# Kernel optimization log

Measured on AMD Instinct MI355X. Metric: run time of the kernel, lower is better.

## Reference

```python
import jax, jax.numpy as jnp
import numpy as np

N_NODES = 50000
N_EDGES = 800000
IN_DIM = 128
HID = 256
B_SEEDS = 8192
EPS = 1e-12


def _sage_layer(h, src, dst, Wn, Ws, b):
    # mean-aggregation SAGEConv: fc_self(h) + fc_neigh(mean over in-neighbors)
    msgs = h[src]  # [E, d]
    agg = jax.ops.segment_sum(msgs, dst, num_segments=N_NODES)
    cnt = jax.ops.segment_sum(jnp.ones((src.shape[0], 1), h.dtype), dst, num_segments=N_NODES)
    neigh = agg / jnp.maximum(cnt, 1.0)
    return neigh @ Wn + h @ Ws + b


def _sage(x, src, dst, Wn1, Ws1, b1, Wn2, Ws2, b2):
    h = jax.nn.relu(_sage_layer(x, src, dst, Wn1, Ws1, b1))
    return _sage_layer(h, src, dst, Wn2, Ws2, b2)


def _l2norm(x):
    # F.normalize(p=2, dim=1)
    n = jnp.sqrt(jnp.sum(x * x, axis=1, keepdims=True))
    return x / jnp.maximum(n, EPS)


def _unique_gather(h, ids):
    # torch.unique(ids, return_inverse=True) then h[inverse]
    uniq, inv = jnp.unique(ids, return_inverse=True, size=ids.shape[0], fill_value=0)
    return h[uniq][inv]


def setup_inputs() -> dict:
    key = jax.random.key(0)
    ks = jax.random.split(key, 16)
    s = lambda d: 1.0 / np.sqrt(d)
    return {
        "x_i": jax.random.normal(ks[0], (N_NODES, IN_DIM), jnp.float32),
        "x_j": jax.random.normal(ks[1], (N_NODES, IN_DIM), jnp.float32),
        "src_i": jax.random.randint(ks[2], (N_EDGES,), 0, N_NODES, jnp.int32),
        "dst_i": jax.random.randint(ks[3], (N_EDGES,), 0, N_NODES, jnp.int32),
        "src_j": jax.random.randint(ks[4], (N_EDGES,), 0, N_NODES, jnp.int32),
        "dst_j": jax.random.randint(ks[5], (N_EDGES,), 0, N_NODES, jnp.int32),
        "ids_i": jax.random.randint(ks[6], (B_SEEDS,), 0, N_NODES, jnp.int32),
        "ids_j": jax.random.randint(ks[7], (B_SEEDS,), 0, N_NODES, jnp.int32),
        "Wn1": jax.random.normal(ks[8], (IN_DIM, HID), jnp.float32) * s(IN_DIM),
        "Ws1": jax.random.normal(ks[9], (IN_DIM, HID), jnp.float32) * s(IN_DIM),
        "b1": jnp.zeros((HID,), jnp.float32),
        "Wn2": jax.random.normal(ks[10], (HID, HID), jnp.float32) * s(HID),
        "Ws2": jax.random.normal(ks[11], (HID, HID), jnp.float32) * s(HID),
        "b2": jnp.zeros((HID,), jnp.float32),
        "W_out": jax.random.normal(ks[12], (2 * HID, 1), jnp.float32) * s(2 * HID),
        "b_out": jnp.zeros((1,), jnp.float32),
    }


def reference(x_i, x_j, src_i, dst_i, src_j, dst_j, ids_i, ids_j,
              Wn1, Ws1, b1, Wn2, Ws2, b2, W_out, b_out):
    sage_o_i = _l2norm(_sage(x_i, src_i, dst_i, Wn1, Ws1, b1, Wn2, Ws2, b2))
    sage_o_j = _l2norm(_sage(x_j, src_j, dst_j, Wn1, Ws1, b1, Wn2, Ws2, b2))
    g_i = _unique_gather(sage_o_i, ids_i)  # [B, HID]
    g_j = _unique_gather(sage_o_j, ids_j)
    h_cur = jnp.concatenate([g_i, g_j], axis=-1) @ W_out + b_out  # [B, 1]
    return jnp.stack([h_cur.squeeze(-1)])  # [1, B]
```

## Files before the change

### kernel.cpp

```cpp
#include <hip/hip_runtime.h>

constexpr int NN = 50000;
constexpr int NE = 800000;
constexpr int IND = 128;
constexpr int HD = 256;
constexpr int BS = 8192;
constexpr int NPAD = 50176;
constexpr int NBKT = 196;
constexpr int BCAP = 8192;

typedef __attribute__((ext_vector_type(8))) short short8v;
typedef __attribute__((ext_vector_type(4))) float floatx4;

__device__ inline ushort f2b(float f) {
  unsigned u = __float_as_uint(f);
  unsigned r = (u + 0x7fffu + ((u >> 16) & 1u)) >> 16;
  return (ushort)r;
}
__device__ inline float b2f(ushort b) {
  return __uint_as_float((unsigned)b << 16);
}
__device__ __forceinline__ void acc2(unsigned u, float& a0, float& a1) {
  a0 += __uint_as_float(u << 16);
  a1 += __uint_as_float(u & 0xffff0000u);
}
__device__ inline int wave_incl_scan(int x, int lane) {
#pragma unroll
  for (int d = 1; d < 64; d <<= 1) {
    int y = __shfl_up(x, d);
    if (lane >= d) x += y;
  }
  return x;
}

__device__ __forceinline__ void gload16(const ushort* g, ushort* l) {
  __builtin_amdgcn_global_load_lds(
      (const __attribute__((address_space(1))) void*)g,
      (__attribute__((address_space(3))) void*)l, 16, 0, 0);
}

__global__ __launch_bounds__(256) void k_bin(const int* __restrict__ src_i,
                                             const int* __restrict__ dst_i,
                                             const int* __restrict__ src_j,
                                             const int* __restrict__ dst_j,
                                             int* __restrict__ bcnt,
                                             int* __restrict__ bucketbuf) {
  __shared__ int hist[NBKT], gbase[NBKT], lcur[NBKT];
  const int blk = blockIdx.x;
  const int g = blk >= 98;
  const int c = blk - g * 98;
  const int* src = g ? src_j : src_i;
  const int* dst = g ? dst_j : dst_i;
  const int t = threadIdx.x;
  if (t < NBKT) hist[t] = 0;
  __syncthreads();
  const int e0 = c * 8192;
#pragma unroll
  for (int k = 0; k < 32; ++k) {
    int e = e0 + k * 256 + t;
    if (e < NE) atomicAdd(&hist[dst[e] >> 8], 1);
  }
  __syncthreads();
  if (t < NBKT) {
    int h = hist[t];
    gbase[t] = h ? atomicAdd(&bcnt[g * NBKT + t], h) : 0;
    lcur[t] = 0;
  }
  __syncthreads();
#pragma unroll
  for (int k = 0; k < 32; ++k) {
    int e = e0 + k * 256 + t;
    if (e < NE) {
      int d = dst[e];
      int b = d >> 8;
      int p = gbase[b] + atomicAdd(&lcur[b], 1);
      if (p < BCAP)
        bucketbuf[(g * NBKT + b) * BCAP + p] = (src[e] << 8) | (d & 255);
    }
  }
}

__global__ __launch_bounds__(256) void k_bktscan(const int* __restrict__ bcnt,
                                                 int* __restrict__ bktbase) {
  __shared__ int wt[4];
  __shared__ int carry, tot;
  const int t = threadIdx.x, lane = t & 63;
  if (t == 0) carry = 0;
  __syncthreads();
  for (int ch = 0; ch < 2; ++ch) {
    int i = ch * 256 + t;
    int v = (i < 2 * NBKT) ? min(bcnt[i], BCAP) : 0;
    int x = wave_incl_scan(v, lane);
    if (lane == 63) wt[t >> 6] = x;
    __syncthreads();
    if (t == 0) {
      int run = 0;
#pragma unroll
      for (int j = 0; j < 4; ++j) { int tv = wt[j]; wt[j] = run; run += tv; }
      tot = run;
    }
    __syncthreads();
    if (i < 2 * NBKT) bktbase[i] = carry + x - v + wt[t >> 6];
    __syncthreads();
    if (t == 0) carry += tot;
    __syncthreads();
  }
}

__global__ __launch_bounds__(256) void k_build(const int* __restrict__ bucketbuf,
                                               const int* __restrict__ bcnt,
                                               const int* __restrict__ bktbase,
                                               int* __restrict__ csr,
                                               int* __restrict__ cnt2,
                                               int* __restrict__ row_start2) {
  __shared__ int hist[256], lstart[256], lcur[256];
  __shared__ int stage[BCAP];
  __shared__ int wt[4];
  const int b = blockIdx.x;
  const int g = b >= NBKT;
  const int bb = b - g * NBKT;
  const int t = threadIdx.x, lane = t & 63;
  const int C = min(bcnt[b], BCAP);
  const int base = bktbase[b];
  const int* buf = bucketbuf + b * BCAP;
  hist[t] = 0;
  __syncthreads();
  for (int i = t; i < C; i += 256) atomicAdd(&hist[buf[i] & 255], 1);
  __syncthreads();
  int v = hist[t];
  int x = wave_incl_scan(v, lane);
  if (lane == 63) wt[t >> 6] = x;
  __syncthreads();
  if (t == 0) {
    int run = 0;
#pragma unroll
    for (int j = 0; j < 4; ++j) { int tv = wt[j]; wt[j] = run; run += tv; }
  }
  __syncthreads();
  int ls = x - v + wt[t >> 6];
  lstart[t] = ls;
  lcur[t] = ls;
  __syncthreads();
  for (int i = t; i < C; i += 256) {
    int val = buf[i];
    int p = atomicAdd(&lcur[val & 255], 1);
    stage[p] = val >> 8;
  }
  __syncthreads();
  for (int i = t; i < C; i += 256) csr[base + i] = stage[i];
  int node = bb * 256 + t;
  cnt2[g * NPAD + node] = v;
  row_start2[g * NPAD + node] = base + ls;
}

__global__ __launch_bounds__(256) void k_tobf16(const float* __restrict__ x_i,
                                                const float* __restrict__ x_j,
                                                ushort* __restrict__ xb2) {
  int i = blockIdx.x * 256 + threadIdx.x;
  int e4 = i * 4;
  int g = e4 >= NN * IND;
  const float* xp = g ? x_j : x_i;
  float4 v = *(const float4*)(xp + (e4 - g * NN * IND));
  ushort4 u;
  u.x = f2b(v.x); u.y = f2b(v.y); u.z = f2b(v.z); u.w = f2b(v.w);
  *(ushort4*)(xb2 + e4) = u;
}

__global__ __launch_bounds__(256) void k_wt(const float* __restrict__ Wn1,
                                            const float* __restrict__ Ws1,
                                            ushort* __restrict__ Wt) {
  int i = blockIdx.x * 256 + threadIdx.x;
  int n = i >> 8, k = i & 255;
  float v = (k < 128) ? Wn1[k * HD + n] : Ws1[(k - 128) * HD + n];
  Wt[n * 256 + k] = f2b(v);
}

__global__ __launch_bounds__(256) void k_w2(const float* __restrict__ Wn2,
                                            const float* __restrict__ Ws2,
                                            ushort* __restrict__ Whi,
                                            ushort* __restrict__ Wlo) {
  int i = blockIdx.x * 256 + threadIdx.x;
  int n = i >> 9, k = i & 511;
  float v = (k < 256) ? Wn2[k * HD + n] : Ws2[(k - 256) * HD + n];
  ushort hi = f2b(v);
  Whi[n * 512 + k] = hi;
  Wlo[n * 512 + k] = f2b(v - b2f(hi));
}

__global__ __launch_bounds__(256) void k_agg1(const ushort* __restrict__ xb2,
                                              const int* __restrict__ csr,
                                              const int* __restrict__ row_start2,
                                              const int* __restrict__ cnt2,
                                              ushort* __restrict__ aggb2) {
  int w = threadIdx.x >> 6, l = threadIdx.x & 63;
  int n = blockIdx.x * 4 + w;
  int g = n >= NN;
  int nl = n - g * NN;
  int st = row_start2[g * NPAD + nl], deg = cnt2[g * NPAD + nl];
  const ushort* xb = xb2 + g * NN * IND;
  float a0 = 0.f, a1 = 0.f;
  int e = 0;
  for (; e + 8 <= deg; e += 8) {
    int s0 = csr[st + e + 0], s1 = csr[st + e + 1];
    int s2 = csr[st + e + 2], s3 = csr[st + e + 3];
    int s4 = csr[st + e + 4], s5 = csr[st + e + 5];
    int s6 = csr[st + e + 6], s7 = csr[st + e + 7];
    unsigned u0 = *(const unsigned*)(xb + s0 * IND + 2 * l);
    unsigned u1 = *(const unsigned*)(xb + s1 * IND + 2 * l);
    unsigned u2 = *(const unsigned*)(xb + s2 * IND + 2 * l);
    unsigned u3 = *(const unsigned*)(xb + s3 * IND + 2 * l);
    unsigned u4 = *(const unsigned*)(xb + s4 * IND + 2 * l);
    unsigned u5 = *(const unsigned*)(xb + s5 * IND + 2 * l);
    unsigned u6 = *(const unsigned*)(xb + s6 * IND + 2 * l);
    unsigned u7 = *(const unsigned*)(xb + s7 * IND + 2 * l);
    acc2(u0, a0, a1); acc2(u1, a0, a1); acc2(u2, a0, a1); acc2(u3, a0, a1);
    acc2(u4, a0, a1); acc2(u5, a0, a1); acc2(u6, a0, a1); acc2(u7, a0, a1);
  }
  for (; e + 4 <= deg; e += 4) {
    int s0 = csr[st + e + 0], s1 = csr[st + e + 1];
    int s2 = csr[st + e + 2], s3 = csr[st + e + 3];
    unsigned u0 = *(const unsigned*)(xb + s0 * IND + 2 * l);
    unsigned u1 = *(const unsigned*)(xb + s1 * IND + 2 * l);
    unsigned u2 = *(const unsigned*)(xb + s2 * IND + 2 * l);
    unsigned u3 = *(const unsigned*)(xb + s3 * IND + 2 * l);
    acc2(u0, a0, a1); acc2(u1, a0, a1); acc2(u2, a0, a1); acc2(u3, a0, a1);
  }
  for (; e < deg; ++e) {
    int s = csr[st + e];
    unsigned u = *(const unsigned*)(xb + s * IND + 2 * l);
    acc2(u, a0, a1);
  }
  float inv = 1.f / (float)max(deg, 1);
  ushort2 u;
  u.x = f2b(a0 * inv);
  u.y = f2b(a1 * inv);
  *(ushort2*)(aggb2 + (g * NN + nl) * IND + 2 * l) = u;
}

__global__ __launch_bounds__(256) void k_gemm1(const ushort* __restrict__ aggb2,
                                               const ushort* __restrict__ xb2,
                                               const ushort* __restrict__ Wt,
                                               const float* __restrict__ b1,
                                               ushort* __restrict__ h1b2) {
  __shared__ ushort smem[16384];
  const int t = threadIdx.x;
  const int g = blockIdx.x >= 392;
  const int row0 = (blockIdx.x - g * 392) * 128, col0 = blockIdx.y * 128;
  const ushort* aggb = aggb2 + g * NN * IND;
  const ushort* xb = xb2 + g * NN * IND;
  ushort* h1b = h1b2 + g * NN * HD;
  const int w = t >> 6, l = t & 63;
  const int wm = w & 1, wn = w >> 1;

  const int r0 = t >> 2, cs0 = t & 3;
  const int c0 = cs0 ^ (r0 & 3);
  const int rA0 = min(row0 + r0, NN - 1);
  const int rA1 = min(row0 + r0 + 64, NN - 1);
  const int gA0 = rA0 * IND + c0 * 8;
  const int gA1 = rA1 * IND + c0 * 8;
  const int gB0 = (col0 + r0) * 256 + c0 * 8;
  const int gB1 = (col0 + r0 + 64) * 256 + c0 * 8;
  const int wofs = w * 512;

  floatx4 acc[4][4];
#pragma unroll
  for (int i = 0; i < 4; ++i)
#pragma unroll
    for (int j = 0; j < 4; ++j) acc[i][j] = (floatx4){0.f, 0.f, 0.f, 0.f};

#define STAGE(buf, kk)                                                      \
  do {                                                                      \
    const ushort* Ab = ((kk) < 128) ? (aggb + (kk)) : (xb + ((kk) - 128));  \
    ushort* Ald = smem + (buf) * 4096;                                      \
    ushort* Bld = smem + 8192 + (buf) * 4096;                               \
    gload16(Ab + gA0, Ald + wofs);                                          \
    gload16(Ab + gA1, Ald + 2048 + wofs);                                   \
    gload16(Wt + gB0 + (kk), Bld + wofs);                                   \
    gload16(Wt + gB1 + (kk), Bld + 2048 + wofs);                            \
  } while (0)

  STAGE(0, 0);
  __syncthreads();
  int cur = 0;
  const int rA = l & 15, gg = l >> 4;
  for (int step = 0; step < 8; ++step) {
    if (step < 7) STAGE(cur ^ 1, (step + 1) * 32);
    const ushort* Abuf = smem + cur * 4096;
    const ushort* Bbuf = smem + 8192 + cur * 4096;
    short8v af[4], bf[4];
#pragma unroll
    for (int i = 0; i < 4; ++i) {
      int r = wm * 64 + i * 16 + rA;
      af[i] = *(const short8v*)(Abuf + r * 32 + ((gg ^ (r & 3)) * 8));
    }
#pragma unroll
    for (int j = 0; j < 4; ++j) {
      int r = wn * 64 + j * 16 + rA;
      bf[j] = *(const short8v*)(Bbuf + r * 32 + ((gg ^ (r & 3)) * 8));
    }
#pragma unroll
    for (int i = 0; i < 4; ++i)
#pragma unroll
      for (int j = 0; j < 4; ++j)
        acc[i][j] = __builtin_amdgcn_mfma_f32_16x16x32_bf16(af[i], bf[j],
                                                            acc[i][j], 0, 0, 0);
    if (step < 7) {
      __syncthreads();
      cur ^= 1;
    }
  }
#undef STAGE

  __syncthreads();
  const int rD = l >> 4, cD = l & 15;
#pragma unroll
  for (int j = 0; j < 4; ++j) {
    int cl = wn * 64 + j * 16 + cD;
    float bias = b1[col0 + cl];
#pragma unroll
    for (int i = 0; i < 4; ++i) {
      int rbase = wm * 64 + i * 16 + rD * 4;
#pragma unroll
      for (int rr = 0; rr < 4; ++rr)
        smem[(rbase + rr) * 128 + cl] = f2b(fmaxf(acc[i][j][rr] + bias, 0.f));
    }
  }
  __syncthreads();
  const int rl = t >> 4, ch = t & 15;
#pragma unroll
  for (int it = 0; it < 8; ++it) {
    int row_l = rl + it * 16;
    int grow = row0 + row_l;
    if (grow < NN)
      *(short8v*)(h1b + grow * HD + col0 + ch * 8) =
          *(const short8v*)(smem + row_l * 128 + ch * 8);
  }
}

__global__ __launch_bounds__(256) void k_agg2(
    const ushort* __restrict__ h1b2, const int* __restrict__ csr,
    const int* __restrict__ row_start2, const int* __restrict__ cnt2,
    const int* __restrict__ ids_i, const int* __restrict__ ids_j,
    ushort* __restrict__ A2) {
  __shared__ float red[4][HD];
  const int b = blockIdx.x;
  const int g = b >= BS;
  const int node = (g ? ids_j : ids_i)[b - g * BS];
  const int st = row_start2[g * NPAD + node], deg = cnt2[g * NPAD + node];
  const ushort* h1b = h1b2 + g * NN * HD;
  const int w = threadIdx.x >> 6, l = threadIdx.x & 63;
  float a0 = 0.f, a1 = 0.f, a2 = 0.f, a3 = 0.f;
  int e = w;
  for (; e + 4 < deg; e += 8) {
    int sa = csr[st + e], sb = csr[st + e + 4];
    uint2 ua = *(const uint2*)(h1b + sa * HD + l * 4);
    uint2 ub = *(const uint2*)(h1b + sb * HD + l * 4);
    acc2(ua.x, a0, a1); acc2(ua.y, a2, a3);
    acc2(ub.x, a0, a1); acc2(ub.y, a2, a3);
  }
  if (e < deg) {
    int sa = csr[st + e];
    uint2 ua = *(const uint2*)(h1b + sa * HD + l * 4);
    acc2(ua.x, a0, a1); acc2(ua.y, a2, a3);
  }
  red[w][l * 4 + 0] = a0;
  red[w][l * 4 + 1] = a1;
  red[w][l * 4 + 2] = a2;
  red[w][l * 4 + 3] = a3;
  __syncthreads();
  const int t = threadIdx.x;
  float s = (red[0][t] + red[1][t]) + (red[2][t] + red[3][t]);
  s *= 1.f / (float)max(deg, 1);
  A2[b * 512 + t] = f2b(s);
  A2[b * 512 + 256 + t] = h1b[node * HD + t];
}

__global__ __launch_bounds__(256) void k_head(const ushort* __restrict__ A2,
                                              const ushort* __restrict__ Whi,
                                              const ushort* __restrict__ Wlo,
                                              const float* __restrict__ b2,
                                              float* __restrict__ h2) {
  __shared__ ushort Ahl[64 * 32];
  __shared__ ushort Bhl[128 * 32];
  __shared__ ushort Bll[128 * 32];
  const int t = threadIdx.x;
  const int row0 = blockIdx.x * 64, col0 = blockIdx.y * 128;
  const int w = t >> 6, l = t & 63;
  const int wm = w & 1, wn = w >> 1;
  floatx4 acc[2][4];
#pragma unroll
  for (int i = 0; i < 2; ++i)
#pragma unroll
    for (int j = 0; j < 4; ++j) acc[i][j] = (floatx4){0.f, 0.f, 0.f, 0.f};

  for (int kk = 0; kk < 512; kk += 32) {
    if (t < 256) {
      int r = t >> 2, c = t & 3;
      int sw = (c ^ (r & 3)) * 8;
      *(short8v*)(Ahl + r * 32 + sw) =
          *(const short8v*)(A2 + (row0 + r) * 512 + kk + c * 8);
    }
#pragma unroll
    for (int s = t; s < 512; s += 256) {
      int r = s >> 2, c = s & 3;
      int sw = (c ^ (r & 3)) * 8;
      *(short8v*)(Bhl + r * 32 + sw) =
          *(const short8v*)(Whi + (col0 + r) * 512 + kk + c * 8);
      *(short8v*)(Bll + r * 32 + sw) =
          *(const short8v*)(Wlo + (col0 + r) * 512 + kk + c * 8);
    }
    __syncthreads();
    const int rA = l & 15, gg = l >> 4;
    short8v ah[2], bh[4], bl[4];
#pragma unroll
    for (int i = 0; i < 2; ++i) {
      int r = wm * 32 + i * 16 + rA;
      ah[i] = *(const short8v*)(Ahl + r * 32 + ((gg ^ (r & 3)) * 8));
    }
#pragma unroll
    for (int j = 0; j < 4; ++j) {
      int r = wn * 64 + j * 16 + rA;
      int sw = (gg ^ (r & 3)) * 8;
      bh[j] = *(const short8v*)(Bhl + r * 32 + sw);
      bl[j] = *(const short8v*)(Bll + r * 32 + sw);
    }
#pragma unroll
    for (int i = 0; i < 2; ++i)
#pragma unroll
      for (int j = 0; j < 4; ++j) {
        acc[i][j] = __builtin_amdgcn_mfma_f32_16x16x32_bf16(ah[i], bh[j],
                                                            acc[i][j], 0, 0, 0);
        acc[i][j] = __builtin_amdgcn_mfma_f32_16x16x32_bf16(ah[i], bl[j],
                                                            acc[i][j], 0, 0, 0);
      }
    __syncthreads();
  }
  const int rD = l >> 4, cD = l & 15;
#pragma unroll
  for (int j = 0; j < 4; ++j) {
    int col = col0 + wn * 64 + j * 16 + cD;
    float bias = b2[col];
#pragma unroll
    for (int i = 0; i < 2; ++i) {
      int rbase = row0 + wm * 32 + i * 16 + rD * 4;
#pragma unroll
      for (int rr = 0; rr < 4; ++rr) {
        h2[(rbase + rr) * HD + col] = acc[i][j][rr] + bias;
      }
    }
  }
}

__global__ __launch_bounds__(256) void k_out(const float* __restrict__ h2,
                                             const float* __restrict__ W_out,
                                             const float* __restrict__ b_out,
                                             float* __restrict__ out) {
  int w = threadIdx.x >> 6, l = threadIdx.x & 63;
  int s = blockIdx.x * 4 + w;
  float4 vi = *(const float4*)(h2 + s * HD + l * 4);
  float4 vj = *(const float4*)(h2 + (s + BS) * HD + l * 4);
  float4 wi = *(const float4*)(W_out + l * 4);
  float4 wj = *(const float4*)(W_out + 256 + l * 4);
  float ssi = vi.x * vi.x + vi.y * vi.y + vi.z * vi.z + vi.w * vi.w;
  float dpi = vi.x * wi.x + vi.y * wi.y + vi.z * wi.z + vi.w * wi.w;
  float ssj = vj.x * vj.x + vj.y * vj.y + vj.z * vj.z + vj.w * vj.w;
  float dpj = vj.x * wj.x + vj.y * wj.y + vj.z * wj.z + vj.w * wj.w;
#pragma unroll
  for (int o = 32; o; o >>= 1) {
    ssi += __shfl_down(ssi, o);
    dpi += __shfl_down(dpi, o);
    ssj += __shfl_down(ssj, o);
    dpj += __shfl_down(dpj, o);
  }
  if (l == 0) {
    out[s] = dpi / fmaxf(sqrtf(ssi), 1e-12f) +
             dpj / fmaxf(sqrtf(ssj), 1e-12f) + b_out[0];
  }
}

extern "C" void kernel_launch(void* const* d_in, const int* in_sizes, int n_in,
                              void* d_out, int out_size, void* d_ws,
                              size_t ws_size, hipStream_t stream) {
  (void)in_sizes; (void)n_in; (void)out_size; (void)ws_size;
  const float* x_i = (const float*)d_in[0];
  const float* x_j = (const float*)d_in[1];
  const int* src_i = (const int*)d_in[2];
  const int* dst_i = (const int*)d_in[3];
  const int* src_j = (const int*)d_in[4];
  const int* dst_j = (const int*)d_in[5];
  const int* ids_i = (const int*)d_in[6];
  const int* ids_j = (const int*)d_in[7];
  const float* Wn1 = (const float*)d_in[8];
  const float* Ws1 = (const float*)d_in[9];
  const float* b1 = (const float*)d_in[10];
  const float* Wn2 = (const float*)d_in[11];
  const float* Ws2 = (const float*)d_in[12];
  const float* b2 = (const float*)d_in[13];
  const float* W_out = (const float*)d_in[14];
  const float* b_out = (const float*)d_in[15];
  float* out = (float*)d_out;

  char* w = (char*)d_ws;
  int* bcnt       = (int*)(w + 0);
  int* bktbase    = (int*)(w + 2048);
  int* cnt2       = (int*)(w + 4096);
  int* row_start2 = (int*)(w + 405504);
  int* bucketbuf  = (int*)(w + 806912);
  ushort* Wt      = (ushort*)(w + 13651968);
  ushort* W2hi    = (ushort*)(w + 13783040);
  ushort* W2lo    = (ushort*)(w + 14045184);
  ushort* xb2     = (ushort*)(w + 14307328);
  ushort* aggb2   = (ushort*)(w + 39907328);
  ushort* h1b2    = (ushort*)(w + 65507328);
  int* csr        = (int*)(w + 116707328);
  ushort* A2      = (ushort*)(w + 14307328);
  float* h2       = (float*)(w + 31084544);

  k_wt<<<256, 256, 0, stream>>>(Wn1, Ws1, Wt);
  k_w2<<<512, 256, 0, stream>>>(Wn2, Ws2, W2hi, W2lo);
  hipMemsetAsync(bcnt, 0, 2 * NBKT * sizeof(int), stream);
  k_bin<<<196, 256, 0, stream>>>(src_i, dst_i, src_j, dst_j, bcnt, bucketbuf);
  k_bktscan<<<1, 256, 0, stream>>>(bcnt, bktbase);
  k_build<<<392, 256, 0, stream>>>(bucketbuf, bcnt, bktbase, csr, cnt2,
                                   row_start2);
  k_tobf16<<<12500, 256, 0, stream>>>(x_i, x_j, xb2);
  k_agg1<<<25000, 256, 0, stream>>>(xb2, csr, row_start2, cnt2, aggb2);
  k_gemm1<<<dim3(784, 2), 256, 0, stream>>>(aggb2, xb2, Wt, b1, h1b2);
  k_agg2<<<2 * BS, 256, 0, stream>>>(h1b2, csr, row_start2, cnt2, ids_i, ids_j,
                                     A2);
  k_head<<<dim3(256, 2), 256, 0, stream>>>(A2, W2hi, W2lo, b2, h2);
  k_out<<<2048, 256, 0, stream>>>(h2, W_out, b_out, out);
}
```

Measured before the change: 211.5 us.

## Fuse weight prep kernels, pair nodes per wave in agg1, fuse L2-norm+output into head GEMM

Merges the two weight-conversion kernels and the bucket memset into one prep launch. Layer-1 aggregation now has each wave handle two nodes, interleaving their gathers so more loads are in flight. The head GEMM now covers all 256 columns per block, so it can compute the L2 norm and the W_out dot product in its epilogue instead of writing h2 and reading it back in a separate kernel. A small kernel then sums the i and j halves. This trades fewer launches and less h2 traffic for a larger per-block tile (more registers and LDS) and only 256 head blocks.

```diff
diff --git a/kernel.cpp b/kernel.cpp
--- a/kernel.cpp
+++ b/kernel.cpp
@@ -37,6 +37,32 @@
   __builtin_amdgcn_global_load_lds(
       (const __attribute__((address_space(1))) void*)g,
       (__attribute__((address_space(3))) void*)l, 16, 0, 0);
+}
+
+__global__ __launch_bounds__(256) void k_prep(const float* __restrict__ Wn1,
+                                              const float* __restrict__ Ws1,
+                                              const float* __restrict__ Wn2,
+                                              const float* __restrict__ Ws2,
+                                              ushort* __restrict__ Wt,
+                                              ushort* __restrict__ Whi,
+                                              ushort* __restrict__ Wlo,
+                                              int* __restrict__ bcnt) {
+  const int b = blockIdx.x, t = threadIdx.x;
+  if (b < 256) {
+    int i = b * 256 + t;
+    int n = i >> 8, k = i & 255;
+    float v = (k < 128) ? Wn1[k * HD + n] : Ws1[(k - 128) * HD + n];
+    Wt[n * 256 + k] = f2b(v);
+  } else if (b < 768) {
+    int i = (b - 256) * 256 + t;
+    int n = i >> 9, k = i & 511;
+    float v = (k < 256) ? Wn2[k * HD + n] : Ws2[(k - 256) * HD + n];
+    ushort hi = f2b(v);
+    Whi[n * 512 + k] = hi;
+    Wlo[n * 512 + k] = f2b(v - b2f(hi));
+  } else {
+    for (int i = t; i < 2 * NBKT; i += 256) bcnt[i] = 0;
+  }
 }
 
 __global__ __launch_bounds__(256) void k_bin(const int* __restrict__ src_i,
@@ -166,75 +192,79 @@
   *(ushort4*)(xb2 + e4) = u;
 }
 
-__global__ __launch_bounds__(256) void k_wt(const float* __restrict__ Wn1,
-                                            const float* __restrict__ Ws1,
-                                            ushort* __restrict__ Wt) {
-  int i = blockIdx.x * 256 + threadIdx.x;
-  int n = i >> 8, k = i & 255;
-  float v = (k < 128) ? Wn1[k * HD + n] : Ws1[(k - 128) * HD + n];
-  Wt[n * 256 + k] = f2b(v);
-}
-
-__global__ __launch_bounds__(256) void k_w2(const float* __restrict__ Wn2,
-                                            const float* __restrict__ Ws2,
-                                            ushort* __restrict__ Whi,
-                                            ushort* __restrict__ Wlo) {
-  int i = blockIdx.x * 256 + threadIdx.x;
-  int n = i >> 9, k = i & 511;
-  float v = (k < 256) ? Wn2[k * HD + n] : Ws2[(k - 256) * HD + n];
-  ushort hi = f2b(v);
-  Whi[n * 512 + k] = hi;
-  Wlo[n * 512 + k] = f2b(v - b2f(hi));
-}
-
 __global__ __launch_bounds__(256) void k_agg1(const ushort* __restrict__ xb2,
                                               const int* __restrict__ csr,
                                               const int* __restrict__ row_start2,
                                               const int* __restrict__ cnt2,
                                               ushort* __restrict__ aggb2) {
   int w = threadIdx.x >> 6, l = threadIdx.x & 63;
-  int n = blockIdx.x * 4 + w;
-  int g = n >= NN;
-  int nl = n - g * NN;
-  int st = row_start2[g * NPAD + nl], deg = cnt2[g * NPAD + nl];
+  int p = blockIdx.x * 4 + w;
+  int nA = p * 2;
+  int g = nA >= NN;
+  int nl = nA - g * NN;
+  int base = g * NPAD + nl;
+  int stA = row_start2[base], degA = cnt2[base];
+  int stB = row_start2[base + 1], degB = cnt2[base + 1];
   const ushort* xb = xb2 + g * NN * IND;
-  float a0 = 0.f, a1 = 0.f;
+  float a0A = 0.f, a1A = 0.f, a0B = 0.f, a1B = 0.f;
+  int cmn = min(degA, degB);
   int e = 0;
-  for (; e + 8 <= deg; e += 8) {
-    int s0 = csr[st + e + 0], s1 = csr[st + e + 1];
-    int s2 = csr[st + e + 2], s3 = csr[st + e + 3];
-    int s4 = csr[st + e + 4], s5 = csr[st + e + 5];
-    int s6 = csr[st + e + 6], s7 = csr[st + e + 7];
+  for (; e + 4 <= cmn; e += 4) {
+    int sA0 = csr[stA + e + 0], sA1 = csr[stA + e + 1];
+    int sA2 = csr[stA + e + 2], sA3 = csr[stA + e + 3];
+    int sB0 = csr[stB + e + 0], sB1 = csr[stB + e + 1];
+    int sB2 = csr[stB + e + 2], sB3 = csr[stB + e + 3];
+    unsigned uA0 = *(const unsigned*)(xb + sA0 * IND + 2 * l);
+    unsigned uA1 = *(const unsigned*)(xb + sA1 * IND + 2 * l);
+    unsigned uA2 = *(const unsigned*)(xb + sA2 * IND + 2 * l);
+    unsigned uA3 = *(const unsigned*)(xb + sA3 * IND + 2 * l);
+    unsigned uB0 = *(const unsigned*)(xb + sB0 * IND + 2 * l);
+    unsigned uB1 = *(const unsigned*)(xb + sB1 * IND + 2 * l);
+    unsigned uB2 = *(const unsigned*)(xb + sB2 * IND + 2 * l);
+    unsigned uB3 = *(const unsigned*)(xb + sB3 * IND + 2 * l);
+    acc2(uA0, a0A, a1A); acc2(uA1, a0A, a1A);
+    acc2(uA2, a0A, a1A); acc2(uA3, a0A, a1A);
+    acc2(uB0, a0B, a1B); acc2(uB1, a0B, a1B);
+    acc2(uB2, a0B, a1B); acc2(uB3, a0B, a1B);
+  }
+  int eA = e, eB = e;
+  for (; eA + 4 <= degA; eA += 4) {
+    int s0 = csr[stA + eA + 0], s1 = csr[stA + eA + 1];
+    int s2 = csr[stA + eA + 2], s3 = csr[stA + eA + 3];
     unsigned u0 = *(const unsigned*)(xb + s0 * IND + 2 * l);
     unsigned u1 = *(const unsigned*)(xb + s1 * IND + 2 * l);
     unsigned u2 = *(const unsigned*)(xb + s2 * IND + 2 * l);
     unsigned u3 = *(const unsigned*)(xb + s3 * IND + 2 * l);
-    unsigned u4 = *(const unsigned*)(xb + s4 * IND + 2 * l);
-    unsigned u5 = *(const unsigned*)(xb + s5 * IND + 2 * l);
-    unsigned u6 = *(const unsigned*)(xb + s6 * IND + 2 * l);
-    unsigned u7 = *(const unsigned*)(xb + s7 * IND + 2 * l);
-    acc2(u0, a0, a1); acc2(u1, a0, a1); acc2(u2, a0, a1); acc2(u3, a0, a1);
-    acc2(u4, a0, a1); acc2(u5, a0, a1); acc2(u6, a0, a1); acc2(u7, a0, a1);
-  }
-  for (; e + 4 <= deg; e += 4) {
-    int s0 = csr[st + e + 0], s1 = csr[st + e + 1];
-    int s2 = csr[st + e + 2], s3 = csr[st + e + 3];
+    acc2(u0, a0A, a1A); acc2(u1, a0A, a1A);
+    acc2(u2, a0A, a1A); acc2(u3, a0A, a1A);
+  }
+  for (; eA < degA; ++eA) {
+    int s = csr[stA + eA];
+    unsigned u = *(const unsigned*)(xb + s * IND + 2 * l);
+    acc2(u, a0A, a1A);
+  }
+  for (; eB + 4 <= degB; eB += 4) {
+    int s0 = csr[stB + eB + 0], s1 = csr[stB + eB + 1];
+    int s2 = csr[stB + eB + 2], s3 = csr[stB + eB + 3];
     unsigned u0 = *(const unsigned*)(xb + s0 * IND + 2 * l);
     unsigned u1 = *(const unsigned*)(xb + s1 * IND + 2 * l);
     unsigned u2 = *(const unsigned*)(xb + s2 * IND + 2 * l);
     unsigned u3 = *(const unsigned*)(xb + s3 * IND + 2 * l);
-    acc2(u0, a0, a1); acc2(u1, a0, a1); acc2(u2, a0, a1); acc2(u3, a0, a1);
-  }
-  for (; e < deg; ++e) {
-    int s = csr[st + e];
+    acc2(u0, a0B, a1B); acc2(u1, a0B, a1B);
+    acc2(u2, a0B, a1B); acc2(u3, a0B, a1B);
+  }
+  for (; eB < degB; ++eB) {
+    int s = csr[stB + eB];
     unsigned u = *(const unsigned*)(xb + s * IND + 2 * l);
-    acc2(u, a0, a1);
-  }
-  float inv = 1.f / (float)max(deg, 1);
-  ushort2 u;
-  u.x = f2b(a0 * inv);
-  u.y = f2b(a1 * inv);
-  *(ushort2*)(aggb2 + (g * NN + nl) * IND + 2 * l) = u;
+    acc2(u, a0B, a1B);
+  }
+  float invA = 1.f / (float)max(degA, 1);
+  float invB = 1.f / (float)max(degB, 1);
+  ushort2 uA, uB;
+  uA.x = f2b(a0A * invA); uA.y = f2b(a1A * invA);
+  uB.x = f2b(a0B * invB); uB.y = f2b(a1B * invB);
+  *(ushort2*)(aggb2 + (g * NN + nl) * IND + 2 * l) = uA;
+  *(ushort2*)(aggb2 + (g * NN + nl + 1) * IND + 2 * l) = uB;
 }
 
 __global__ __launch_bounds__(256) void k_gemm1(const ushort* __restrict__ aggb2,
@@ -379,103 +409,107 @@
                                               const ushort* __restrict__ Whi,
                                               const ushort* __restrict__ Wlo,
                                               const float* __restrict__ b2,
-                                              float* __restrict__ h2) {
+                                              const float* __restrict__ W_out,
+                                              float* __restrict__ outP) {
   __shared__ ushort Ahl[64 * 32];
-  __shared__ ushort Bhl[128 * 32];
-  __shared__ ushort Bll[128 * 32];
+  __shared__ ushort Bhl[256 * 32];
+  __shared__ ushort Bll[256 * 32];
+  __shared__ float sred[4][64][2];
   const int t = threadIdx.x;
-  const int row0 = blockIdx.x * 64, col0 = blockIdx.y * 128;
+  const int row0 = blockIdx.x * 64;
   const int w = t >> 6, l = t & 63;
-  const int wm = w & 1, wn = w >> 1;
-  floatx4 acc[2][4];
-#pragma unroll
-  for (int i = 0; i < 2; ++i)
+  const int woff = (row0 >= BS) ? 256 : 0;
+  floatx4 acc[4][4];
+#pragma unroll
+  for (int i = 0; i < 4; ++i)
 #pragma unroll
     for (int j = 0; j < 4; ++j) acc[i][j] = (floatx4){0.f, 0.f, 0.f, 0.f};
 
   for (int kk = 0; kk < 512; kk += 32) {
-    if (t < 256) {
+    {
       int r = t >> 2, c = t & 3;
       int sw = (c ^ (r & 3)) * 8;
       *(short8v*)(Ahl + r * 32 + sw) =
           *(const short8v*)(A2 + (row0 + r) * 512 + kk + c * 8);
     }
 #pragma unroll
-    for (int s = t; s < 512; s += 256) {
+    for (int s = t; s < 1024; s += 256) {
       int r = s >> 2, c = s & 3;
       int sw = (c ^ (r & 3)) * 8;
       *(short8v*)(Bhl + r * 32 + sw) =
-          *(const short8v*)(Whi + (col0 + r) * 512 + kk + c * 8);
+          *(const short8v*)(Whi + r * 512 + kk + c * 8);
       *(short8v*)(Bll + r * 32 + sw) =
-          *(const short8v*)(Wlo + (col0 + r) * 512 + kk + c * 8);
+          *(const short8v*)(Wlo + r * 512 + kk + c * 8);
     }
     __syncthreads();
     const int rA = l & 15, gg = l >> 4;
-    short8v ah[2], bh[4], bl[4];
-#pragma unroll
-    for (int i = 0; i < 2; ++i) {
-      int r = wm * 32 + i * 16 + rA;
-      ah[i] = *(const short8v*)(Ahl + r * 32 + ((gg ^ (r & 3)) * 8));
+    short8v af[4], bh[4], bl[4];
+#pragma unroll
+    for (int i = 0; i < 4; ++i) {
+      int r = i * 16 + rA;
+      af[i] = *(const short8v*)(Ahl + r * 32 + ((gg ^ (r & 3)) * 8));
     }
 #pragma unroll
     for (int j = 0; j < 4; ++j) {
-      int r = wn * 64 + j * 16 + rA;
+      int r = w * 64 + j * 16 + rA;
       int sw = (gg ^ (r & 3)) * 8;
       bh[j] = *(const short8v*)(Bhl + r * 32 + sw);
       bl[j] = *(const short8v*)(Bll + r * 32 + sw);
     }
 #pragma unroll
-    for (int i = 0; i < 2; ++i)
+    for (int i = 0; i < 4; ++i)
 #pragma unroll
       for (int j = 0; j < 4; ++j) {
-        acc[i][j] = __builtin_amdgcn_mfma_f32_16x16x32_bf16(ah[i], bh[j],
+        acc[i][j] = __builtin_amdgcn_mfma_f32_16x16x32_bf16(af[i], bh[j],
                                                             acc[i][j], 0, 0, 0);
-        acc[i][j] = __builtin_amdgcn_mfma_f32_16x16x32_bf16(ah[i], bl[j],
+        acc[i][j] = __builtin_amdgcn_mfma_f32_16x16x32_bf16(af[i], bl[j],
                                                             acc[i][j], 0, 0, 0);
       }
     __syncthreads();
   }
-  const int rD = l >> 4, cD = l & 15;
+  const int cD = l & 15, rD = l >> 4;
+  float bj[4], wo[4];
 #pragma unroll
   for (int j = 0; j < 4; ++j) {
-    int col = col0 + wn * 64 + j * 16 + cD;
-    float bias = b2[col];
-#pragma unroll
-    for (int i = 0; i < 2; ++i) {
-      int rbase = row0 + wm * 32 + i * 16 + rD * 4;
-#pragma unroll
-      for (int rr = 0; rr < 4; ++rr) {
-        h2[(rbase + rr) * HD + col] = acc[i][j][rr] + bias;
+    int col = w * 64 + j * 16 + cD;
+    bj[j] = b2[col];
+    wo[j] = W_out[woff + col];
+  }
+#pragma unroll
+  for (int i = 0; i < 4; ++i)
+#pragma unroll
+    for (int rr = 0; rr < 4; ++rr) {
+      float ssv = 0.f, dpv = 0.f;
+#pragma unroll
+      for (int j = 0; j < 4; ++j) {
+        float v = acc[i][j][rr] + bj[j];
+        ssv += v * v;
+        dpv += v * wo[j];
       }
-    }
-  }
-}
-
-__global__ __launch_bounds__(256) void k_out(const float* __restrict__ h2,
-                                             const float* __restrict__ W_out,
-                                             const float* __restrict__ b_out,
-                                             float* __restrict__ out) {
-  int w = threadIdx.x >> 6, l = threadIdx.x & 63;
-  int s = blockIdx.x * 4 + w;
-  float4 vi = *(const float4*)(h2 + s * HD + l * 4);
-  float4 vj = *(const float4*)(h2 + (s + BS) * HD + l * 4);
-  float4 wi = *(const float4*)(W_out + l * 4);
-  float4 wj = *(const float4*)(W_out + 256 + l * 4);
-  float ssi = vi.x * vi.x + vi.y * vi.y + vi.z * vi.z + vi.w * vi.w;
-  float dpi = vi.x * wi.x + vi.y * wi.y + vi.z * wi.z + vi.w * wi.w;
-  float ssj = vj.x * vj.x + vj.y * vj.y + vj.z * vj.z + vj.w * vj.w;
-  float dpj = vj.x * wj.x + vj.y * wj.y + vj.z * wj.z + vj.w * wj.w;
-#pragma unroll
-  for (int o = 32; o; o >>= 1) {
-    ssi += __shfl_down(ssi, o);
-    dpi += __shfl_down(dpi, o);
-    ssj += __shfl_down(ssj, o);
-    dpj += __shfl_down(dpj, o);
-  }
-  if (l == 0) {
-    out[s] = dpi / fmaxf(sqrtf(ssi), 1e-12f) +
-             dpj / fmaxf(sqrtf(ssj), 1e-12f) + b_out[0];
-  }
+#pragma unroll
+      for (int d = 1; d < 16; d <<= 1) {
+        ssv += __shfl_xor(ssv, d);
+        dpv += __shfl_xor(dpv, d);
+      }
+      if (cD == 0) {
+        int row = i * 16 + rD * 4 + rr;
+        sred[w][row][0] = ssv;
+        sred[w][row][1] = dpv;
+      }
+    }
+  __syncthreads();
+  if (t < 64) {
+    float ss = (sred[0][t][0] + sred[1][t][0]) + (sred[2][t][0] + sred[3][t][0]);
+    float dp = (sred[0][t][1] + sred[1][t][1]) + (sred[2][t][1] + sred[3][t][1]);
+    outP[row0 + t] = dp / fmaxf(sqrtf(ss), 1e-12f);
+  }
+}
+
+__global__ __launch_bounds__(256) void k_out2(const float* __restrict__ outP,
+                                              const float* __restrict__ b_out,
+                                              float* __restrict__ out) {
+  int s = blockIdx.x * 256 + threadIdx.x;
+  if (s < BS) out[s] = outP[s] + outP[s + BS] + b_out[0];
 }
 
 extern "C" void kernel_launch(void* const* d_in, const int* in_sizes, int n_in,
@@ -514,20 +548,18 @@
   ushort* h1b2    = (ushort*)(w + 65507328);
   int* csr        = (int*)(w + 116707328);
   ushort* A2      = (ushort*)(w + 14307328);
-  float* h2       = (float*)(w + 31084544);
-
-  k_wt<<<256, 256, 0, stream>>>(Wn1, Ws1, Wt);
-  k_w2<<<512, 256, 0, stream>>>(Wn2, Ws2, W2hi, W2lo);
-  hipMemsetAsync(bcnt, 0, 2 * NBKT * sizeof(int), stream);
+  float* outP     = (float*)(w + 31084544);
+
+  k_prep<<<769, 256, 0, stream>>>(Wn1, Ws1, Wn2, Ws2, Wt, W2hi, W2lo, bcnt);
   k_bin<<<196, 256, 0, stream>>>(src_i, dst_i, src_j, dst_j, bcnt, bucketbuf);
   k_bktscan<<<1, 256, 0, stream>>>(bcnt, bktbase);
   k_build<<<392, 256, 0, stream>>>(bucketbuf, bcnt, bktbase, csr, cnt2,
                                    row_start2);
   k_tobf16<<<12500, 256, 0, stream>>>(x_i, x_j, xb2);
-  k_agg1<<<25000, 256, 0, stream>>>(xb2, csr, row_start2, cnt2, aggb2);
+  k_agg1<<<12500, 256, 0, stream>>>(xb2, csr, row_start2, cnt2, aggb2);
   k_gemm1<<<dim3(784, 2), 256, 0, stream>>>(aggb2, xb2, Wt, b1, h1b2);
   k_agg2<<<2 * BS, 256, 0, stream>>>(h1b2, csr, row_start2, cnt2, ids_i, ids_j,
                                      A2);
-  k_head<<<dim3(256, 2), 256, 0, stream>>>(A2, W2hi, W2lo, b2, h2);
-  k_out<<<2048, 256, 0, stream>>>(h2, W_out, b_out, out);
-}
+  k_head<<<256, 256, 0, stream>>>(A2, W2hi, W2lo, b2, W_out, outP);
+  k_out2<<<32, 256, 0, stream>>>(outP, b_out, out);
+}
```

After: 211.8 us. Within noise of the previous version (+0.2%).
